# Performance work log

Hardware: AMD Instinct MI355X
Metric: run time of the kernel (lower is better)

The kernel has to match this reference:

```python
import jax, jax.numpy as jnp
import numpy as np
import math

H, W = 1024, 1024

def setup_inputs() -> dict:
    key = jax.random.key(0)
    img = jax.random.uniform(key, (H, W), dtype=jnp.float32) * 255.0
    return {"InputImage": img}

def _phase_congruency(img):
    nrows, ncols = img.shape
    minWaveLength, mult = 3.0, 2.1
    nscale, norient = 5, 6
    sigmaOnf, k, cutOff, g = 0.55, 2.0, 0.5, 10.0
    eps = 1e-4

    cy, cx = nrows // 2, ncols // 2
    yy, xx = jnp.mgrid[0:nrows, 0:ncols]
    yy = (yy - cy) / nrows
    xx = (xx - cx) / ncols
    radius = jnp.sqrt(xx ** 2 + yy ** 2)
    radius = radius.at[cy, cx].set(1.0)
    theta = jnp.arctan2(-yy, xx)
    sintheta, costheta = jnp.sin(theta), jnp.cos(theta)

    # low-pass Butterworth (order 15, cutoff 0.45)
    normradius = radius / (jnp.abs(xx).max() * 2)
    lowpass = 1.0 / (1.0 + (normradius / 0.45) ** 30)

    # log-Gabor radial filters, [nscale, H, W]
    s = jnp.arange(nscale, dtype=jnp.float32)
    fo = 1.0 / (minWaveLength * mult ** s)            # [S]
    logGabor = jnp.exp(-jnp.log(radius[None] * (1.0 / fo)[:, None, None]) ** 2
                       / (2 * math.log(sigmaOnf) ** 2))
    annular = logGabor * lowpass[None]
    annular = annular.at[:, cy, cx].set(0.0)

    # angular spread, [norient, H, W]
    angl = jnp.arange(norient, dtype=jnp.float32) * (math.pi / norient)
    cosA, sinA = jnp.cos(angl), jnp.sin(angl)
    ds = sintheta[None] * cosA[:, None, None] - costheta[None] * sinA[:, None, None]
    dc = costheta[None] * cosA[:, None, None] + sintheta[None] * sinA[:, None, None]
    dtheta = jnp.minimum(jnp.abs(jnp.arctan2(ds, dc)) * (norient / 2), math.pi)
    spread = (jnp.cos(dtheta) + 1.0) / 2.0

    # full filter bank [O, S, H, W], shifted to DFT layout
    filt = jnp.fft.ifftshift(spread[:, None] * annular[None], axes=(-2, -1))

    F = jnp.fft.fft2(img)                              # complex64
    # cv2.idft is unscaled -> multiply numpy-style ifft by N
    z = jnp.fft.ifft2(filt * F[None, None]) * (nrows * ncols)   # [O,S,H,W]
    # original code: E (even) = channel 1 = Im(z), O (odd) = channel 0 = Re(z)
    E, O = z.imag, z.real
    An = jnp.abs(z)

    sumE = E.sum(axis=1)        # [O,H,W]
    sumO = O.sum(axis=1)
    sumAn = An.sum(axis=1)
    maxAn = An.max(axis=1)
    tau = jnp.median(An[:, 0].reshape(norient, -1), axis=1) / math.sqrt(math.log(4.0))

    XEnergy = jnp.sqrt(sumE ** 2 + sumO ** 2) + eps
    MeanE = sumE / XEnergy
    MeanO = sumO / XEnergy
    Energy = (E * MeanE[:, None] + O * MeanO[:, None]
              - jnp.abs(E * MeanO[:, None] - O * MeanE[:, None])).sum(axis=1)

    totalTau = tau * (1 - (1 / mult) ** nscale) / (1 - 1 / mult)   # [O]
    T = totalTau * math.sqrt(math.pi / 2) + k * totalTau * math.sqrt((4 - math.pi) / 2)
    Energy = jnp.maximum(Energy - T[:, None, None], 0.0)

    width = (sumAn / (maxAn + eps) - 1.0) / (nscale - 1)
    weight = 1.0 / (1.0 + jnp.exp((cutOff - width) * g))
    PC = weight * Energy / sumAn                       # [O,H,W]

    covx = PC * cosA[:, None, None]
    covy = PC * sinA[:, None, None]
    covx2 = (covx ** 2).sum(axis=0) / (norient / 2)
    covy2 = (covy ** 2).sum(axis=0) / (norient / 2)
    covxy = 4.0 * (covx * covy).sum(axis=0) / norient
    denom = jnp.sqrt(covxy ** 2 + (covx2 - covy2) ** 2) + eps
    M = (covy2 + covx2 + denom) / 2.0
    m = (covy2 + covx2 - denom) / 2.0
    return M, m

def reference(InputImage):
    M, m = _phase_congruency(InputImage)
    return (M, m)
```

## Files before the change

kernel.cpp:

```cpp
#include <hip/hip_runtime.h>
#include <math.h>

typedef float2 c2;

#define S_IDX(i) ((i) ^ (((i) >> 5) & 15))

__device__ __forceinline__ c2 cmul(c2 a, c2 b){
  return make_float2(a.x*b.x - a.y*b.y, a.x*b.y + a.y*b.x);
}

__constant__ float c_lnfo[5]  = {1.0986123f, 1.8405496f, 2.5824700f, 3.3244106f, 4.0663219f};
__constant__ float c_angl[6]  = {0.0f, 0.5235988f, 1.0471976f, 1.5707963f, 2.0943951f, 2.6179939f};
__constant__ float c_cosA[6] = {1.0f, 0.8660254038f, 0.5f, 6.123233996e-17f, -0.5f, -0.8660254038f};
__constant__ float c_sinA[6] = {0.0f, 0.5f, 0.8660254038f, 1.0f, 0.8660254038f, 0.5f};

template<int SIGN>
__device__ __forceinline__ void make_tw(int t, c2* w){
#pragma unroll
  for (int k = 0; k < 5; ++k){
    const int s = 1 << (2*k);
    const float ang = (float)SIGN * 0.00613592315154256f * (float)(t & ~(s-1));
    sincosf(ang, &w[k].y, &w[k].x);
  }
}

template<int SIGN>
__device__ __forceinline__ void fft1024(c2* bufA, c2* bufB, int t, const c2* w){
  c2* cur = bufA; c2* oth = bufB;
#pragma unroll
  for (int k = 0; k < 5; ++k){
    const int s = 1 << (2*k);
    const int q = t & (s - 1);
    c2 a = cur[S_IDX(t)];
    c2 b = cur[S_IDX(t + 256)];
    c2 c = cur[S_IDX(t + 512)];
    c2 d = cur[S_IDX(t + 768)];
    c2 w1 = w[k];
    c2 w2 = cmul(w1, w1);
    c2 w3 = cmul(w2, w1);
    c2 apc = make_float2(a.x + c.x, a.y + c.y);
    c2 amc = make_float2(a.x - c.x, a.y - c.y);
    c2 bpd = make_float2(b.x + d.x, b.y + d.y);
    c2 bmd = make_float2(b.x - d.x, b.y - d.y);
    c2 y0 = make_float2(apc.x + bpd.x, apc.y + bpd.y);
    c2 e2 = make_float2(apc.x - bpd.x, apc.y - bpd.y);
    const float S4 = (float)SIGN;
    c2 u1 = make_float2(amc.x - S4*bmd.y, amc.y + S4*bmd.x);
    c2 u3 = make_float2(amc.x + S4*bmd.y, amc.y - S4*bmd.x);
    c2 y1 = cmul(u1, w1);
    c2 y2 = cmul(e2, w2);
    c2 y3 = cmul(u3, w3);
    const int bw = 4*t - 3*q;
    oth[S_IDX(bw)]       = y0;
    oth[S_IDX(bw + s)]   = y1;
    oth[S_IDX(bw + 2*s)] = y2;
    oth[S_IDX(bw + 3*s)] = y3;
    c2* tmp = cur; cur = oth; oth = tmp;
    __syncthreads();
  }
}

__global__ __launch_bounds__(256) void k_filt_tab(float* __restrict__ lnrT, float* __restrict__ thetaT){
  const int a = blockIdx.x;
  const int t = threadIdx.x;
  const float xx = (float)(a < 512 ? a : a - 1024) * (1.0f/1024.0f);
#pragma unroll
  for (int j = 0; j < 4; ++j){
    const int q = t + 256*j;
    const float yy = (float)(q < 512 ? q : q - 1024) * (1.0f/1024.0f);
    const float radius = sqrtf(xx*xx + yy*yy);
    float lnr = logf(radius);
    if (a == 0 && q == 0) lnr = __int_as_float(0x7F800000);
    lnrT[a*1024 + q] = lnr;
    thetaT[a*1024 + q] = atan2f(-yy, xx);
  }
}

__global__ __launch_bounds__(256) void k_fft_fwd_real(const float* __restrict__ in, c2* __restrict__ out){
  const int t = threadIdx.x;
  __shared__ c2 bufA[1024];
  __shared__ c2 bufB[1024];
  c2 w[5]; make_tw<-1>(t, w);
  for (int rr = 0; rr < 4; ++rr){
    const int row = blockIdx.x * 4 + rr;
    const float* src = in + (size_t)row * 1024;
    c2* dst = out + (size_t)row * 1024;
#pragma unroll
    for (int j = 0; j < 4; ++j){
      const int q = t + 256*j;
      bufA[S_IDX(q)] = make_float2(src[q], 0.0f);
    }
    __syncthreads();
    fft1024<-1>(bufA, bufB, t, w);
#pragma unroll
    for (int j = 0; j < 4; ++j){ const int q = t + 256*j; dst[q] = bufB[S_IDX(q)]; }
    __syncthreads();
  }
}

__global__ __launch_bounds__(256) void k_fft_fwd_ip(c2* __restrict__ Z){
  const int t = threadIdx.x;
  c2* base = Z + (size_t)blockIdx.y * 1048576;
  __shared__ c2 bufA[1024];
  __shared__ c2 bufB[1024];
  c2 w[5]; make_tw<-1>(t, w);
  for (int rr = 0; rr < 4; ++rr){
    const int row = blockIdx.x * 4 + rr;
    c2* p = base + (size_t)row * 1024;
#pragma unroll
    for (int j = 0; j < 4; ++j){ const int q = t + 256*j; bufA[S_IDX(q)] = p[q]; }
    __syncthreads();
    fft1024<-1>(bufA, bufB, t, w);
#pragma unroll
    for (int j = 0; j < 4; ++j){ const int q = t + 256*j; p[q] = bufB[S_IDX(q)]; }
    __syncthreads();
  }
}

__global__ __launch_bounds__(256) void k_fft_inv_filter_g(const c2* __restrict__ F, c2* __restrict__ Z,
                                                          const float* __restrict__ lnrT,
                                                          const float* __restrict__ thetaT, int orient0){
  const int t = threadIdx.x;
  const int orient = orient0 + blockIdx.y;
  const float angl = c_angl[orient];
  __shared__ c2 bufA[1024];
  __shared__ c2 bufB[1024];
  __shared__ c2 Frow[1024];
  __shared__ float commSh[1024];
  __shared__ float lnrSh[1024];
  c2 w[5]; make_tw<1>(t, w);
  for (int rr = 0; rr < 4; ++rr){
    const int row = blockIdx.x * 4 + rr;
    const c2* src = F + (size_t)row * 1024;
    const float* lnrR = lnrT + (size_t)row * 1024;
    const float* thR  = thetaT + (size_t)row * 1024;
#pragma unroll
    for (int j = 0; j < 4; ++j){
      const int q = t + 256*j;
      Frow[q] = src[q];
      const float lnr = lnrR[q];
      const float th  = thR[q];
      const float lp = 1.0f/(1.0f + __expf(fmaf(30.f, lnr, 23.955231f)));
      float d = th - angl;
      if (d <= -3.14159274f) d += 6.28318548f;
      const float dth = fminf(fabsf(d)*3.0f, 3.14159274f);
      const float spr = 0.5f*(__cosf(dth)+1.0f);
      lnrSh[q] = lnr;
      commSh[q] = lp*spr;
    }
    __syncthreads();
    for (int s = 0; s < 5; ++s){
      const float lnfo = c_lnfo[s];
      c2* dst = Z + ((size_t)blockIdx.y*5 + s) * 1048576 + (size_t)row * 1024;
#pragma unroll
      for (int j = 0; j < 4; ++j){
        const int q = t + 256*j;
        const float u = lnrSh[q] + lnfo;
        const float f = __expf(-u*u*1.3989572f) * commSh[q];
        const c2 v = Frow[q];
        bufA[S_IDX(q)] = make_float2(v.x*f, v.y*f);
      }
      __syncthreads();
      fft1024<1>(bufA, bufB, t, w);
#pragma unroll
      for (int j = 0; j < 4; ++j){ const int q = t + 256*j; dst[q] = bufB[S_IDX(q)]; }
      __syncthreads();
    }
  }
}

__global__ __launch_bounds__(256) void k_fft_inv_ip(c2* __restrict__ Z){
  const int t = threadIdx.x;
  c2* base = Z + (size_t)blockIdx.y * 1048576;
  __shared__ c2 bufA[1024];
  __shared__ c2 bufB[1024];
  c2 w[5]; make_tw<1>(t, w);
  for (int rr = 0; rr < 4; ++rr){
    const int row = blockIdx.x * 4 + rr;
    c2* p = base + (size_t)row * 1024;
#pragma unroll
    for (int j = 0; j < 4; ++j){ const int q = t + 256*j; bufA[S_IDX(q)] = p[q]; }
    __syncthreads();
    fft1024<1>(bufA, bufB, t, w);
#pragma unroll
    for (int j = 0; j < 4; ++j){ const int q = t + 256*j; p[q] = bufB[S_IDX(q)]; }
    __syncthreads();
  }
}

__global__ void k_transpose_ip(c2* __restrict__ Zb){
  __shared__ c2 A[32][33];
  __shared__ c2 B[32][33];
  c2* base = Zb + (size_t)blockIdx.y * 1048576;
  const int p = blockIdx.x;
  int i = (int)floorf((sqrtf(8.0f*(float)p + 1.0f) - 1.0f) * 0.5f);
  while ((i+1)*(i+2)/2 <= p) ++i;
  while (i*(i+1)/2 > p) --i;
  const int j = p - i*(i+1)/2;
  const int tx = threadIdx.x, ty = threadIdx.y;
  const int r0 = i*32, c0 = j*32;
#pragma unroll
  for (int jj = 0; jj < 32; jj += 8)
    A[ty+jj][tx] = base[(size_t)(r0+ty+jj)*1024 + c0+tx];
  if (i != j){
#pragma unroll
    for (int jj = 0; jj < 32; jj += 8)
      B[ty+jj][tx] = base[(size_t)(c0+ty+jj)*1024 + r0+tx];
  }
  __syncthreads();
#pragma unroll
  for (int jj = 0; jj < 32; jj += 8)
    base[(size_t)(c0+ty+jj)*1024 + r0+tx] = A[tx][ty+jj];
  if (i != j){
#pragma unroll
    for (int jj = 0; jj < 32; jj += 8)
      base[(size_t)(r0+ty+jj)*1024 + c0+tx] = B[tx][ty+jj];
  }
}


__device__ __forceinline__ unsigned amp_bits(const c2 v){
  return __float_as_uint(sqrtf(v.x*v.x + v.y*v.y));
}

__global__ __launch_bounds__(256) void k_med_p1b(const c2* __restrict__ Zb, size_t oStride,
                                                 unsigned* __restrict__ g1, int oBase){
  __shared__ unsigned h[4][4096];
  const int t = threadIdx.x;
  const int wv = t >> 6;
  const c2* z0 = Zb + (size_t)blockIdx.y * oStride;
  unsigned* gg = g1 + (size_t)(oBase + blockIdx.y) * 4096;
  for (int j = t; j < 4*4096; j += 256) ((unsigned*)h)[j] = 0;
  __syncthreads();
  const int base = blockIdx.x * 16384;
  for (int it = 0; it < 64; ++it){
    const unsigned bits = amp_bits(z0[base + it*256 + t]);
    atomicAdd(&h[wv][bits >> 20], 1u);
  }
  __syncthreads();
  for (int j = t; j < 4096; j += 256){
    const unsigned s = h[0][j] + h[1][j] + h[2][j] + h[3][j];
    if (s) atomicAdd(&gg[j], s);
  }
}

__global__ __launch_bounds__(256) void k_sel1b(const unsigned* __restrict__ g1,
                                               unsigned* __restrict__ sc1,
                                               unsigned* __restrict__ g2, int oBase){
  __shared__ unsigned partial[256];
  const int t = threadIdx.x;
  const int oo = oBase + blockIdx.x;
  const unsigned* gg = g1 + (size_t)oo * 4096;
  unsigned loc[16]; unsigned s = 0;
#pragma unroll
  for (int j = 0; j < 16; ++j){ loc[j] = gg[t*16 + j]; s += loc[j]; }
  partial[t] = s;
  __syncthreads();
  unsigned p = 0;
  for (int u = 0; u < t; ++u) p += partial[u];
  for (int which = 0; which < 2; ++which){
    const unsigned R = 524287u + (unsigned)which;
    if (R >= p && R - p < s){
      unsigned cum = p;
      for (int j = 0; j < 16; ++j){
        if (R - cum < loc[j]){ sc1[oo*4 + which*2] = (unsigned)(t*16 + j); sc1[oo*4 + which*2+1] = R - cum; break; }
        cum += loc[j];
      }
    }
  }
  for (int j = t; j < 8192; j += 256) g2[(size_t)oo*8192 + j] = 0;
}

__global__ __launch_bounds__(256) void k_med_p2b(const c2* __restrict__ Zb, size_t oStride,
                                                 const unsigned* __restrict__ sc1,
                                                 unsigned* __restrict__ g2, int oBase){
  __shared__ unsigned h[2][4096];
  const int t = threadIdx.x;
  const int oo = oBase + blockIdx.y;
  const c2* z0 = Zb + (size_t)blockIdx.y * oStride;
  unsigned* gg = g2 + (size_t)oo * 8192;
  for (int j = t; j < 8192; j += 256) ((unsigned*)h)[j] = 0;
  __syncthreads();
  const unsigned b0 = sc1[oo*4 + 0], b1 = sc1[oo*4 + 2];
  const int base = blockIdx.x * 16384;
  for (int it = 0; it < 64; ++it){
    const unsigned bits = amp_bits(z0[base + it*256 + t]);
    const unsigned top = bits >> 20;
    const unsigned mid = (bits >> 8) & 4095u;
    if (top == b0)      atomicAdd(&h[0][mid], 1u);
    else if (top == b1) atomicAdd(&h[1][mid], 1u);
  }
  __syncthreads();
  for (int j = t; j < 4096; j += 256){
    if (h[0][j]) atomicAdd(&gg[j], h[0][j]);
    if (h[1][j]) atomicAdd(&gg[4096 + j], h[1][j]);
  }
}

__global__ __launch_bounds__(256) void k_sel2b(const unsigned* __restrict__ g2,
                                               const unsigned* __restrict__ sc1,
                                               unsigned* __restrict__ sc2,
                                               unsigned* __restrict__ g3, int oBase){
  __shared__ unsigned partial[256];
  const int t = threadIdx.x;
  const int oo = oBase + blockIdx.x;
  const unsigned b0 = sc1[oo*4+0], lr0 = sc1[oo*4+1], b1 = sc1[oo*4+2], lr1 = sc1[oo*4+3];
  for (int which = 0; which < 2; ++which){
    const unsigned* hh = g2 + (size_t)oo*8192 + ((which == 1 && b1 != b0) ? 4096 : 0);
    const unsigned R = which ? lr1 : lr0;
    unsigned loc[16]; unsigned s = 0;
#pragma unroll
    for (int j = 0; j < 16; ++j){ loc[j] = hh[t*16 + j]; s += loc[j]; }
    partial[t] = s;
    __syncthreads();
    unsigned p = 0;
    for (int u = 0; u < t; ++u) p += partial[u];
    if (R >= p && R - p < s){
      unsigned cum = p;
      for (int j = 0; j < 16; ++j){
        if (R - cum < loc[j]){ sc2[oo*4 + which*2] = (unsigned)(t*16 + j); sc2[oo*4 + which*2+1] = R - cum; break; }
        cum += loc[j];
      }
    }
    __syncthreads();
  }
  for (int j = t; j < 512; j += 256) g3[(size_t)oo*512 + j] = 0;
}

__global__ __launch_bounds__(256) void k_med_p3b(const c2* __restrict__ Zb, size_t oStride,
                                                 const unsigned* __restrict__ sc1,
                                                 const unsigned* __restrict__ sc2,
                                                 unsigned* __restrict__ g3, int oBase){
  __shared__ unsigned h[2][256];
  const int t = threadIdx.x;
  const int oo = oBase + blockIdx.y;
  const c2* z0 = Zb + (size_t)blockIdx.y * oStride;
  unsigned* gg = g3 + (size_t)oo * 512;
  h[0][t] = 0; h[1][t] = 0;
  __syncthreads();
  const unsigned k0 = (sc1[oo*4+0] << 12) | sc2[oo*4+0];
  const unsigned k1 = (sc1[oo*4+2] << 12) | sc2[oo*4+2];
  const int base = blockIdx.x * 16384;
  for (int it = 0; it < 64; ++it){
    const unsigned bits = amp_bits(z0[base + it*256 + t]);
    const unsigned key = bits >> 8;
    if (key == k0)       atomicAdd(&h[0][bits & 255u], 1u);
    else if (key == k1)  atomicAdd(&h[1][bits & 255u], 1u);
  }
  __syncthreads();
  if (h[0][t]) atomicAdd(&gg[t], h[0][t]);
  if (h[1][t]) atomicAdd(&gg[256 + t], h[1][t]);
}

__global__ __launch_bounds__(256) void k_sel3b(const unsigned* __restrict__ g3,
                                               const unsigned* __restrict__ sc1,
                                               const unsigned* __restrict__ sc2,
                                               float* __restrict__ Tval, int oBase){
  __shared__ unsigned partial[256];
  __shared__ float vres[2];
  const int t = threadIdx.x;
  const int oo = oBase + blockIdx.x;
  const unsigned k0 = (sc1[oo*4+0] << 12) | sc2[oo*4+0];
  const unsigned k1 = (sc1[oo*4+2] << 12) | sc2[oo*4+2];
  for (int which = 0; which < 2; ++which){
    const unsigned* hh = g3 + (size_t)oo*512 + ((which == 1 && k1 != k0) ? 256 : 0);
    const unsigned R = which ? sc2[oo*4+3] : sc2[oo*4+1];
    partial[t] = hh[t];
    __syncthreads();
    unsigned p = 0;
    for (int u = 0; u < t; ++u) p += partial[u];
    if (R >= p && R - p < partial[t]){
      const unsigned key = which ? k1 : k0;
      vres[which] = __uint_as_float((key << 8) | (unsigned)t);
    }
    __syncthreads();
  }
  if (t == 0){
    const float med = 0.5f * (vres[0] + vres[1]);
    const float tau = med / 1.17741001f;
    const float totalTau = tau * 1.8623464f;
    const float T = totalTau * 1.25331414f + 2.0f * totalTau * 0.65513638f;
    Tval[oo] = T;
  }
}


__global__ __launch_bounds__(256) void k_pix_all(const c2* __restrict__ Z, const float* __restrict__ Tval,
                                                 float* __restrict__ out){
  const int i = blockIdx.x * 256 + threadIdx.x;
  float covx2 = 0.f, covy2 = 0.f, covxy = 0.f;
#pragma unroll
  for (int o = 0; o < 6; ++o){
    const float T = Tval[o];
    float E[5], O[5];
    float sumE = 0.f, sumO = 0.f, sumAn = 0.f, maxAn = 0.f;
#pragma unroll
    for (int s = 0; s < 5; ++s){
      const c2 z = Z[(size_t)(o*5 + s) * 1048576 + i];
      O[s] = z.x; E[s] = z.y;
      const float an = sqrtf(z.x*z.x + z.y*z.y);
      sumE += E[s]; sumO += O[s]; sumAn += an; maxAn = fmaxf(maxAn, an);
    }
    const float XE = sqrtf(sumE*sumE + sumO*sumO) + 1e-4f;
    const float ME = sumE / XE, MO = sumO / XE;
    float energy = 0.f;
#pragma unroll
    for (int s = 0; s < 5; ++s)
      energy += E[s]*ME + O[s]*MO - fabsf(E[s]*MO - O[s]*ME);
    energy = fmaxf(energy - T, 0.f);
    const float width = (sumAn / (maxAn + 1e-4f) - 1.0f) * 0.25f;
    const float weight = 1.0f / (1.0f + expf((0.5f - width) * 10.0f));
    const float PC = weight * energy / sumAn;
    const float cx = PC * c_cosA[o], cy = PC * c_sinA[o];
    covx2 += cx*cx; covy2 += cy*cy; covxy += cx*cy;
  }
  covx2 *= (1.0f/3.0f);
  covy2 *= (1.0f/3.0f);
  covxy *= (4.0f/6.0f);
  const float dnm = sqrtf(covxy*covxy + (covx2 - covy2)*(covx2 - covy2)) + 1e-4f;
  const float ss = covy2 + covx2;
  out[i] = (ss + dnm) / 2.0f;
  out[1048576 + i] = (ss - dnm) / 2.0f;
}


__global__ __launch_bounds__(256) void k_pix(const c2* __restrict__ Z, const float* __restrict__ Tp,
                                             float cA, float sA,
                                             float* __restrict__ ax2, float* __restrict__ ay2,
                                             float* __restrict__ axy, int first){
  const int i = blockIdx.x * 256 + threadIdx.x;
  const float T = *Tp;
  float E[5], O[5];
  float sumE = 0.f, sumO = 0.f, sumAn = 0.f, maxAn = 0.f;
#pragma unroll
  for (int s = 0; s < 5; ++s){
    const c2 z = Z[(size_t)s * 1048576 + i];
    O[s] = z.x; E[s] = z.y;
    const float an = sqrtf(z.x*z.x + z.y*z.y);
    sumE += E[s]; sumO += O[s]; sumAn += an; maxAn = fmaxf(maxAn, an);
  }
  const float XE = sqrtf(sumE*sumE + sumO*sumO) + 1e-4f;
  const float ME = sumE / XE, MO = sumO / XE;
  float energy = 0.f;
#pragma unroll
  for (int s = 0; s < 5; ++s)
    energy += E[s]*ME + O[s]*MO - fabsf(E[s]*MO - O[s]*ME);
  energy = fmaxf(energy - T, 0.f);
  const float width = (sumAn / (maxAn + 1e-4f) - 1.0f) * 0.25f;
  const float weight = 1.0f / (1.0f + expf((0.5f - width) * 10.0f));
  const float PC = weight * energy / sumAn;
  const float cx = PC * cA, cy = PC * sA;
  if (first){ ax2[i] = cx*cx; ay2[i] = cy*cy; axy[i] = cx*cy; }
  else      { ax2[i] += cx*cx; ay2[i] += cy*cy; axy[i] += cx*cy; }
}

__global__ __launch_bounds__(256) void k_final(const float* __restrict__ ax2, const float* __restrict__ ay2,
                                               const float* __restrict__ axy, float* __restrict__ out){
  const int i = blockIdx.x * 256 + threadIdx.x;
  const float cx2 = ax2[i] / 3.0f;
  const float cy2 = ay2[i] / 3.0f;
  const float cxy = 4.0f * axy[i] / 6.0f;
  const float dnm = sqrtf(cxy*cxy + (cx2 - cy2)*(cx2 - cy2)) + 1e-4f;
  const float ss = cy2 + cx2;
  out[i] = (ss + dnm) / 2.0f;
  out[1048576 + i] = (ss - dnm) / 2.0f;
}

extern "C" void kernel_launch(void* const* d_in, const int* in_sizes, int n_in,
                              void* d_out, int out_size, void* d_ws, size_t ws_size,
                              hipStream_t stream){
  (void)in_sizes; (void)n_in; (void)out_size;
  const float* img = (const float*)d_in[0];
  float* out = (float*)d_out;
  char* w = (char*)d_ws;

  const dim3 th(256);
  const dim3 thT(32, 8);

  if (ws_size >= (size_t)268435456){
    c2* F  = (c2*)(w);
    c2* Z  = (c2*)(w + 8388608);
    float* lnrT   = (float*)(w + 260046848);
    float* thetaT = (float*)(w + 264241152);
    unsigned* g1  = (unsigned*)(w);
    unsigned* g2  = (unsigned*)(w + 98304);
    unsigned* g3  = (unsigned*)(w + 294912);
    unsigned* sc1 = (unsigned*)(w + 307200);
    unsigned* sc2 = (unsigned*)(w + 307328);
    float* Tval   = (float*)(w + 307456);

    k_filt_tab<<<dim3(1024), th, 0, stream>>>(lnrT, thetaT);

    k_fft_fwd_real<<<dim3(256), th, 0, stream>>>(img, F);
    k_transpose_ip<<<dim3(528, 1), thT, 0, stream>>>(F);
    k_fft_fwd_ip<<<dim3(256, 1), th, 0, stream>>>(F);

    k_fft_inv_filter_g<<<dim3(256, 6), th, 0, stream>>>(F, Z, lnrT, thetaT, 0);
    k_transpose_ip<<<dim3(528, 30), thT, 0, stream>>>(Z);
    k_fft_inv_ip<<<dim3(256, 30), th, 0, stream>>>(Z);

    hipMemsetAsync(g1, 0, 6*16384, stream);
    const size_t oStride = (size_t)5 * 1048576;
    k_med_p1b<<<dim3(64, 6), th, 0, stream>>>(Z, oStride, g1, 0);
    k_sel1b<<<dim3(6), th, 0, stream>>>(g1, sc1, g2, 0);
    k_med_p2b<<<dim3(64, 6), th, 0, stream>>>(Z, oStride, sc1, g2, 0);
    k_sel2b<<<dim3(6), th, 0, stream>>>(g2, sc1, sc2, g3, 0);
    k_med_p3b<<<dim3(64, 6), th, 0, stream>>>(Z, oStride, sc1, sc2, g3, 0);
    k_sel3b<<<dim3(6), th, 0, stream>>>(g3, sc1, sc2, Tval, 0);

    k_pix_all<<<dim3(4096), th, 0, stream>>>(Z, Tval, out);
  } else {
    c2* F   = (c2*)(w);
    c2* C5  = (c2*)(w + 8388608);
    float* lnrT   = (float*)(w + 50331648);
    float* thetaT = (float*)(w + 54525952);
    float* ax2 = (float*)(w + 58720256);
    float* ay2 = ax2 + 1048576;
    float* axy = ay2 + 1048576;
    unsigned* g1  = (unsigned*)(w + 71303168);
    unsigned* g2  = (unsigned*)(w + 71319552);
    unsigned* g3  = (unsigned*)(w + 71352320);
    unsigned* sc1 = (unsigned*)(w + 71354368);
    unsigned* sc2 = (unsigned*)(w + 71354496);
    float* Tval   = (float*)(w + 71354624);

    k_filt_tab<<<dim3(1024), th, 0, stream>>>(lnrT, thetaT);
    k_fft_fwd_real<<<dim3(256), th, 0, stream>>>(img, F);
    k_transpose_ip<<<dim3(528, 1), thT, 0, stream>>>(F);
    k_fft_fwd_ip<<<dim3(256, 1), th, 0, stream>>>(F);

    for (int o = 0; o < 6; ++o){
      k_fft_inv_filter_g<<<dim3(256, 1), th, 0, stream>>>(F, C5, lnrT, thetaT, o);
      k_transpose_ip<<<dim3(528, 5), thT, 0, stream>>>(C5);
      k_fft_inv_ip<<<dim3(256, 5), th, 0, stream>>>(C5);

      hipMemsetAsync(g1, 0, 16384, stream);
      k_med_p1b<<<dim3(64, 1), th, 0, stream>>>(C5, 0, g1, 0);
      k_sel1b<<<dim3(1), th, 0, stream>>>(g1, sc1, g2, 0);
      k_med_p2b<<<dim3(64, 1), th, 0, stream>>>(C5, 0, sc1, g2, 0);
      k_sel2b<<<dim3(1), th, 0, stream>>>(g2, sc1, sc2, g3, 0);
      k_med_p3b<<<dim3(64, 1), th, 0, stream>>>(C5, 0, sc1, sc2, g3, 0);
      k_sel3b<<<dim3(1), th, 0, stream>>>(g3, sc1, sc2, Tval, 0);

      const double a = (double)o * (M_PI/6.0);
      k_pix<<<dim3(4096), th, 0, stream>>>(C5, Tval, (float)cos(a), (float)sin(a),
                                           ax2, ay2, axy, (o == 0) ? 1 : 0);
    }
    k_final<<<dim3(4096), th, 0, stream>>>(ax2, ay2, axy, out);
  }
}
```

Baseline: 417.1 us.

## Fuse first median histogram pass into inverse column FFT; precompute twiddle powers

The first-pass amplitude histogram used for the median is now built inside the final inverse FFT kernel, for the scale-0 slices only. This removes the separate k_med_p1b launch, which re-read the scale-0 planes from memory. Twiddle squares and cubes are also computed once per thread and not in every radix-4 stage. In exchange the FFT kernel uses 16 KB more shared memory (which can lower occupancy), takes shared atomics on the write-out path for one slot in five, and keeps more registers live.

```diff
diff --git a/kernel.cpp b/kernel.cpp
--- a/kernel.cpp
+++ b/kernel.cpp
@@ -15,17 +15,20 @@
 __constant__ float c_sinA[6] = {0.0f, 0.5f, 0.8660254038f, 1.0f, 0.8660254038f, 0.5f};
 
 template<int SIGN>
-__device__ __forceinline__ void make_tw(int t, c2* w){
+__device__ __forceinline__ void make_tw3(int t, c2* w1, c2* w2, c2* w3){
 #pragma unroll
   for (int k = 0; k < 5; ++k){
     const int s = 1 << (2*k);
     const float ang = (float)SIGN * 0.00613592315154256f * (float)(t & ~(s-1));
-    sincosf(ang, &w[k].y, &w[k].x);
+    sincosf(ang, &w1[k].y, &w1[k].x);
+    w2[k] = cmul(w1[k], w1[k]);
+    w3[k] = cmul(w2[k], w1[k]);
   }
 }
 
 template<int SIGN>
-__device__ __forceinline__ void fft1024(c2* bufA, c2* bufB, int t, const c2* w){
+__device__ __forceinline__ void fft1024(c2* bufA, c2* bufB, int t,
+                                        const c2* w1a, const c2* w2a, const c2* w3a){
   c2* cur = bufA; c2* oth = bufB;
 #pragma unroll
   for (int k = 0; k < 5; ++k){
@@ -35,9 +38,6 @@
     c2 b = cur[S_IDX(t + 256)];
     c2 c = cur[S_IDX(t + 512)];
     c2 d = cur[S_IDX(t + 768)];
-    c2 w1 = w[k];
-    c2 w2 = cmul(w1, w1);
-    c2 w3 = cmul(w2, w1);
     c2 apc = make_float2(a.x + c.x, a.y + c.y);
     c2 amc = make_float2(a.x - c.x, a.y - c.y);
     c2 bpd = make_float2(b.x + d.x, b.y + d.y);
@@ -47,9 +47,9 @@
     const float S4 = (float)SIGN;
     c2 u1 = make_float2(amc.x - S4*bmd.y, amc.y + S4*bmd.x);
     c2 u3 = make_float2(amc.x + S4*bmd.y, amc.y - S4*bmd.x);
-    c2 y1 = cmul(u1, w1);
-    c2 y2 = cmul(e2, w2);
-    c2 y3 = cmul(u3, w3);
+    c2 y1 = cmul(u1, w1a[k]);
+    c2 y2 = cmul(e2, w2a[k]);
+    c2 y3 = cmul(u3, w3a[k]);
     const int bw = 4*t - 3*q;
     oth[S_IDX(bw)]       = y0;
     oth[S_IDX(bw + s)]   = y1;
@@ -80,7 +80,7 @@
   const int t = threadIdx.x;
   __shared__ c2 bufA[1024];
   __shared__ c2 bufB[1024];
-  c2 w[5]; make_tw<-1>(t, w);
+  c2 w1[5], w2[5], w3[5]; make_tw3<-1>(t, w1, w2, w3);
   for (int rr = 0; rr < 4; ++rr){
     const int row = blockIdx.x * 4 + rr;
     const float* src = in + (size_t)row * 1024;
@@ -91,7 +91,7 @@
       bufA[S_IDX(q)] = make_float2(src[q], 0.0f);
     }
     __syncthreads();
-    fft1024<-1>(bufA, bufB, t, w);
+    fft1024<-1>(bufA, bufB, t, w1, w2, w3);
 #pragma unroll
     for (int j = 0; j < 4; ++j){ const int q = t + 256*j; dst[q] = bufB[S_IDX(q)]; }
     __syncthreads();
@@ -103,14 +103,14 @@
   c2* base = Z + (size_t)blockIdx.y * 1048576;
   __shared__ c2 bufA[1024];
   __shared__ c2 bufB[1024];
-  c2 w[5]; make_tw<-1>(t, w);
+  c2 w1[5], w2[5], w3[5]; make_tw3<-1>(t, w1, w2, w3);
   for (int rr = 0; rr < 4; ++rr){
     const int row = blockIdx.x * 4 + rr;
     c2* p = base + (size_t)row * 1024;
 #pragma unroll
     for (int j = 0; j < 4; ++j){ const int q = t + 256*j; bufA[S_IDX(q)] = p[q]; }
     __syncthreads();
-    fft1024<-1>(bufA, bufB, t, w);
+    fft1024<-1>(bufA, bufB, t, w1, w2, w3);
 #pragma unroll
     for (int j = 0; j < 4; ++j){ const int q = t + 256*j; p[q] = bufB[S_IDX(q)]; }
     __syncthreads();
@@ -128,7 +128,7 @@
   __shared__ c2 Frow[1024];
   __shared__ float commSh[1024];
   __shared__ float lnrSh[1024];
-  c2 w[5]; make_tw<1>(t, w);
+  c2 w1[5], w2[5], w3[5]; make_tw3<1>(t, w1, w2, w3);
   for (int rr = 0; rr < 4; ++rr){
     const int row = blockIdx.x * 4 + rr;
     const c2* src = F + (size_t)row * 1024;
@@ -161,7 +161,7 @@
         bufA[S_IDX(q)] = make_float2(v.x*f, v.y*f);
       }
       __syncthreads();
-      fft1024<1>(bufA, bufB, t, w);
+      fft1024<1>(bufA, bufB, t, w1, w2, w3);
 #pragma unroll
       for (int j = 0; j < 4; ++j){ const int q = t + 256*j; dst[q] = bufB[S_IDX(q)]; }
       __syncthreads();
@@ -169,22 +169,40 @@
   }
 }
 
-__global__ __launch_bounds__(256) void k_fft_inv_ip(c2* __restrict__ Z){
-  const int t = threadIdx.x;
-  c2* base = Z + (size_t)blockIdx.y * 1048576;
+__device__ __forceinline__ unsigned amp_bits(const c2 v){
+  return __float_as_uint(sqrtf(v.x*v.x + v.y*v.y));
+}
+
+__global__ __launch_bounds__(256) void k_fft_inv_ip_h(c2* __restrict__ Z, unsigned* __restrict__ g1){
+  const int t = threadIdx.x;
+  const int slot = blockIdx.y;
+  const int orient = slot / 5;
+  const bool doHist = (slot - orient*5) == 0;
+  c2* base = Z + (size_t)slot * 1048576;
   __shared__ c2 bufA[1024];
   __shared__ c2 bufB[1024];
-  c2 w[5]; make_tw<1>(t, w);
+  __shared__ unsigned hist[4096];
+  if (doHist) for (int j = t; j < 4096; j += 256) hist[j] = 0;
+  c2 w1[5], w2[5], w3[5]; make_tw3<1>(t, w1, w2, w3);
   for (int rr = 0; rr < 4; ++rr){
     const int row = blockIdx.x * 4 + rr;
     c2* p = base + (size_t)row * 1024;
 #pragma unroll
     for (int j = 0; j < 4; ++j){ const int q = t + 256*j; bufA[S_IDX(q)] = p[q]; }
     __syncthreads();
-    fft1024<1>(bufA, bufB, t, w);
-#pragma unroll
-    for (int j = 0; j < 4; ++j){ const int q = t + 256*j; p[q] = bufB[S_IDX(q)]; }
-    __syncthreads();
+    fft1024<1>(bufA, bufB, t, w1, w2, w3);
+#pragma unroll
+    for (int j = 0; j < 4; ++j){
+      const int q = t + 256*j;
+      const c2 v = bufB[S_IDX(q)];
+      p[q] = v;
+      if (doHist) atomicAdd(&hist[amp_bits(v) >> 20], 1u);
+    }
+    __syncthreads();
+  }
+  if (doHist){
+    for (int j = t; j < 4096; j += 256)
+      if (hist[j]) atomicAdd(&g1[(size_t)orient*4096 + j], hist[j]);
   }
 }
 
@@ -219,10 +237,6 @@
 }
 
 
-__device__ __forceinline__ unsigned amp_bits(const c2 v){
-  return __float_as_uint(sqrtf(v.x*v.x + v.y*v.y));
-}
-
 __global__ __launch_bounds__(256) void k_med_p1b(const c2* __restrict__ Zb, size_t oStride,
                                                  unsigned* __restrict__ g1, int oBase){
   __shared__ unsigned h[4][4096];
@@ -496,12 +510,11 @@
     k_fft_fwd_ip<<<dim3(256, 1), th, 0, stream>>>(F);
 
     k_fft_inv_filter_g<<<dim3(256, 6), th, 0, stream>>>(F, Z, lnrT, thetaT, 0);
+    hipMemsetAsync(g1, 0, 6*16384, stream);
     k_transpose_ip<<<dim3(528, 30), thT, 0, stream>>>(Z);
-    k_fft_inv_ip<<<dim3(256, 30), th, 0, stream>>>(Z);
-
-    hipMemsetAsync(g1, 0, 6*16384, stream);
+    k_fft_inv_ip_h<<<dim3(256, 30), th, 0, stream>>>(Z, g1);
+
     const size_t oStride = (size_t)5 * 1048576;
-    k_med_p1b<<<dim3(64, 6), th, 0, stream>>>(Z, oStride, g1, 0);
     k_sel1b<<<dim3(6), th, 0, stream>>>(g1, sc1, g2, 0);
     k_med_p2b<<<dim3(64, 6), th, 0, stream>>>(Z, oStride, sc1, g2, 0);
     k_sel2b<<<dim3(6), th, 0, stream>>>(g2, sc1, sc2, g3, 0);
@@ -531,11 +544,10 @@
 
     for (int o = 0; o < 6; ++o){
       k_fft_inv_filter_g<<<dim3(256, 1), th, 0, stream>>>(F, C5, lnrT, thetaT, o);
+      hipMemsetAsync(g1, 0, 16384, stream);
       k_transpose_ip<<<dim3(528, 5), thT, 0, stream>>>(C5);
-      k_fft_inv_ip<<<dim3(256, 5), th, 0, stream>>>(C5);
-
-      hipMemsetAsync(g1, 0, 16384, stream);
-      k_med_p1b<<<dim3(64, 1), th, 0, stream>>>(C5, 0, g1, 0);
+      k_fft_inv_ip_h<<<dim3(256, 5), th, 0, stream>>>(C5, g1);
+
       k_sel1b<<<dim3(1), th, 0, stream>>>(g1, sc1, g2, 0);
       k_med_p2b<<<dim3(64, 1), th, 0, stream>>>(C5, 0, sc1, g2, 0);
       k_sel2b<<<dim3(1), th, 0, stream>>>(g2, sc1, sc2, g3, 0);
```

Measured after the change: 398.5 us. 1.05x faster.
